# Kernel tuning notes

Hardware: AMD Instinct MI355X
Metric: run time of the kernel (lower is better)

The kernel has to match this reference:

```python
import jax, jax.numpy as jnp
import numpy as np

HID = 256
NUM_ENT = 100000
NUM_REL = 50
E = 320000  # edges per direction; edge_index has 2*E columns
BN_EPS = 1e-5


def setup_inputs() -> dict:
    key = jax.random.key(0)
    ks = jax.random.split(key, 10)
    x = jax.random.normal(ks[0], (NUM_ENT, HID), dtype=jnp.float32)
    edge_index = jax.random.randint(ks[1], (2, 2 * E), 0, NUM_ENT)
    edge_type = jax.random.randint(ks[2], (2 * E,), 0, NUM_REL)
    rel_embed = jax.random.normal(ks[3], (NUM_REL, HID), dtype=jnp.float32)
    # xavier_normal init: std = sqrt(2 / (fan_in + fan_out))
    w_std = (2.0 / (HID + HID)) ** 0.5
    w_loop = jax.random.normal(ks[4], (HID, HID), dtype=jnp.float32) * w_std
    w_in = jax.random.normal(ks[5], (HID, HID), dtype=jnp.float32) * w_std
    w_out = jax.random.normal(ks[6], (HID, HID), dtype=jnp.float32) * w_std
    w_rel = jax.random.normal(ks[7], (HID, HID), dtype=jnp.float32) * w_std
    loop_rel = jax.random.normal(ks[8], (1, HID), dtype=jnp.float32) * ((2.0 / (1 + HID)) ** 0.5)
    bn_weight = jnp.ones((HID,), dtype=jnp.float32)
    bn_bias = jnp.zeros((HID,), dtype=jnp.float32)
    return {
        "x": x, "edge_index": edge_index, "edge_type": edge_type,
        "rel_embed": rel_embed, "w_loop": w_loop, "w_in": w_in,
        "w_out": w_out, "w_rel": w_rel, "loop_rel": loop_rel,
        "bn_weight": bn_weight, "bn_bias": bn_bias,
    }


def _compute_norm(edge_index, num_ent):
    # symmetric D^-1/2 * D^-1/2 norm; degree counted on row (target) index
    row, col = edge_index[0], edge_index[1]
    deg = jax.ops.segment_sum(jnp.ones_like(row, dtype=jnp.float32), row, num_segments=num_ent)
    deg_inv = jnp.where(deg > 0, deg ** -0.5, 0.0)
    return deg_inv[row] * deg_inv[col]


def _propagate(x, idx, etype, rel_all, W, norm, num_ent):
    # gather source nodes (idx[1]), compose with relation emb (mult), transform, scale, scatter-add to targets (idx[0])
    msg = (x[idx[1]] * rel_all[etype]) @ W  # [E, d]
    if norm is not None:
        msg = msg * norm[:, None]
    return jax.ops.segment_sum(msg, idx[0], num_segments=num_ent)


def reference(x, edge_index, edge_type, rel_embed, w_loop, w_in, w_out, w_rel,
              loop_rel, bn_weight, bn_bias):
    num_ent = x.shape[0]
    rel_all = jnp.concatenate([rel_embed, loop_rel], axis=0)  # [R+1, d]
    e = edge_index.shape[1] // 2
    in_index, out_index = edge_index[:, :e], edge_index[:, e:]
    in_type, out_type = edge_type[:e], edge_type[e:]

    in_norm = _compute_norm(in_index, num_ent)
    out_norm = _compute_norm(out_index, num_ent)

    in_res = _propagate(x, in_index, in_type, rel_all, w_in, in_norm, num_ent)
    out_res = _propagate(x, out_index, out_type, rel_all, w_out, out_norm, num_ent)
    # self-loop: identity scatter -> just per-node compose+transform
    loop_res = (x * loop_rel) @ w_loop

    out = (in_res + out_res + loop_res) * (1.0 / 3.0)

    # BatchNorm1d in training mode (batch stats, biased variance)
    mean = out.mean(axis=0)
    var = out.var(axis=0)
    out = (out - mean) * jax.lax.rsqrt(var + BN_EPS) * bn_weight + bn_bias

    rel_out = (rel_all @ w_rel)[:-1]  # drop loop relation
    return out, rel_out
```

## Files before the change

kernel.cpp:

```cpp
#include <hip/hip_runtime.h>

#define HID     256
#define N_ENT   100000
#define TOT_E   640000
#define HALF_E  320000
#define NSEG    (2 * N_ENT)
#define BN_EPSF 1e-5f
#define SCAN_ELEMS 1024
#define NBLK_SCAN  ((NSEG + SCAN_ELEMS - 1) / SCAN_ELEMS)

typedef short bf16x8 __attribute__((ext_vector_type(8)));
typedef float f32x4  __attribute__((ext_vector_type(4)));

__device__ __forceinline__ short f2b(float f) {
    union { float f; unsigned u; } c; c.f = f;
    unsigned u = c.u;
    u += 0x7FFF + ((u >> 16) & 1);
    return (short)(u >> 16);
}

__global__ void hist_kernel(const int* __restrict__ ei, int* __restrict__ offs) {
    int j = blockIdx.x * 256 + threadIdx.x;
    if (j >= TOT_E) return;
    int seg = ei[j] + ((j < HALF_E) ? 0 : N_ENT);
    atomicAdd(&offs[seg], 1);
}

__global__ __launch_bounds__(256) void scan1(int* __restrict__ offs, int* __restrict__ bsums) {
    __shared__ int tsum[256];
    int b = blockIdx.x, t = threadIdx.x;
    int base = b * SCAN_ELEMS + t * 4;
    int v[4] = {0, 0, 0, 0};
    if (base + 3 < NSEG) {
        int4 lv = *(const int4*)(offs + base);
        v[0] = lv.x; v[1] = lv.y; v[2] = lv.z; v[3] = lv.w;
    } else {
        for (int i = 0; i < 4; ++i) if (base + i < NSEG) v[i] = offs[base + i];
    }
    tsum[t] = v[0] + v[1] + v[2] + v[3];
    __syncthreads();
    for (int d = 1; d < 256; d <<= 1) {
        int val = (t >= d) ? tsum[t - d] : 0;
        __syncthreads();
        tsum[t] += val;
        __syncthreads();
    }
    int run = (t == 0) ? 0 : tsum[t - 1];
    if (t == 255) bsums[b] = tsum[255];
    int w[4];
    for (int i = 0; i < 4; ++i) { w[i] = run; run += v[i]; }
    if (base + 3 < NSEG) *(int4*)(offs + base) = make_int4(w[0], w[1], w[2], w[3]);
    else for (int i = 0; i < 4; ++i) if (base + i < NSEG) offs[base + i] = w[i];
}

__global__ void scan2(int* __restrict__ bsums) {
    __shared__ int tmp[256];
    int t = threadIdx.x;
    int v = (t < NBLK_SCAN) ? bsums[t] : 0;
    tmp[t] = v;
    __syncthreads();
    for (int d = 1; d < 256; d <<= 1) {
        int val = (t >= d) ? tmp[t - d] : 0;
        __syncthreads();
        tmp[t] += val;
        __syncthreads();
    }
    if (t < NBLK_SCAN) bsums[t] = (t == 0) ? 0 : tmp[t - 1];
}

__global__ __launch_bounds__(256) void scan3(int* __restrict__ offs, const int* __restrict__ bsums) {
    int b = blockIdx.x;
    int add = bsums[b];
    int base = b * SCAN_ELEMS + threadIdx.x * 4;
    if (base + 3 < NSEG) {
        int4 v = *(int4*)(offs + base);
        v.x += add; v.y += add; v.z += add; v.w += add;
        *(int4*)(offs + base) = v;
    } else {
        for (int i = 0; i < 4; ++i) if (base + i < NSEG) offs[base + i] += add;
    }
}

__global__ void fill_kernel(const int* __restrict__ ei, const int* __restrict__ et,
                            int* __restrict__ offs, int* __restrict__ elist) {
    int j = blockIdx.x * 256 + threadIdx.x;
    if (j >= TOT_E) return;
    int seg = ei[j] + ((j < HALF_E) ? 0 : N_ENT);
    int pos = atomicAdd(&offs[seg], 1);
    elist[pos] = ei[TOT_E + j] | (et[j] << 17);
}

__global__ __launch_bounds__(256) void gather_kernel(
        const float* __restrict__ x, const float* __restrict__ rel,
        const int* __restrict__ offs, const int* __restrict__ elist,
        float* __restrict__ accA, float* __restrict__ accB) {
    int s = blockIdx.x * 4 + (threadIdx.x >> 6);
    int lane = threadIdx.x & 63;
    int start = (s == 0) ? 0 : offs[s - 1];
    int end   = offs[s];
    int half_base = (s >= N_ENT) ? N_ENT : 0;
    int r = s - half_base;
    float4 a = make_float4(0.f, 0.f, 0.f, 0.f);
    if (end > start) {
        float inv_r = rsqrtf((float)(end - start));
        for (int e = start; e < end; ++e) {
            int p = elist[e];
            int c = p & 0x1FFFF;
            int t = p >> 17;
            int sc = half_base + c;
            int cs = (sc == 0) ? 0 : offs[sc - 1];
            int ce = offs[sc];
            if (ce > cs) {
                float norm = inv_r * rsqrtf((float)(ce - cs));
                float4 xv = *(const float4*)(x   + (size_t)c * HID + lane * 4);
                float4 rv = *(const float4*)(rel + (size_t)t * HID + lane * 4);
                a.x += xv.x * rv.x * norm;
                a.y += xv.y * rv.y * norm;
                a.z += xv.z * rv.z * norm;
                a.w += xv.w * rv.w * norm;
            }
        }
    }
    float* dst = ((s >= N_ENT) ? accB : accA) + (size_t)r * HID + lane * 4;
    *(float4*)dst = a;
}

__global__ void wcat_kernel(const float* __restrict__ w_in, const float* __restrict__ w_out,
                            const float* __restrict__ w_loop, const float* __restrict__ loop_rel,
                            short* __restrict__ WT) {
    int n = blockIdx.x;
    int t = threadIdx.x;
    float v0 = w_in  [(size_t)t * HID + n];
    float v1 = w_out [(size_t)t * HID + n];
    float v2 = w_loop[(size_t)t * HID + n] * loop_rel[t];
    short* row = WT + (size_t)n * 768;
    row[t]       = f2b(v0);
    row[256 + t] = f2b(v1);
    row[512 + t] = f2b(v2);
}

__global__ __launch_bounds__(256) void gemm_mfma(
        const float* __restrict__ accA, const float* __restrict__ accB,
        const float* __restrict__ x, const short* __restrict__ WT,
        float* __restrict__ out, float* __restrict__ stats)
{
    __shared__ __align__(16) short As[64 * 64];
    __shared__ __align__(16) short Bs[256 * 64];
    const int tid = threadIdx.x;
    const int l   = tid & 63;
    const int wid = tid >> 6;
    const int r0  = blockIdx.x * 64;
    const int lr  = l & 15;
    const int lg  = l >> 4;

    f32x4 acc[4][4];
    #pragma unroll
    for (int i = 0; i < 4; ++i)
        #pragma unroll
        for (int j = 0; j < 4; ++j)
            acc[i][j] = (f32x4){0.f, 0.f, 0.f, 0.f};

    const int sg = tid & 7;
    const int sr = tid >> 3;

    for (int kt = 0; kt < 12; ++kt) {
        const int src = kt >> 2;
        const float* Ap = (src == 0) ? accA : ((src == 1) ? accB : x);
        const int ksg = kt * 64;
        const int ksl = (kt & 3) * 64;
        __syncthreads();
        #pragma unroll
        for (int h = 0; h < 2; ++h) {
            int r  = sr + 32 * h;
            int gr = r0 + r;
            float4 v0 = make_float4(0.f,0.f,0.f,0.f), v1 = v0;
            if (gr < N_ENT) {
                const float* p = Ap + (size_t)gr * HID + ksl + sg * 8;
                v0 = *(const float4*)p;
                v1 = *(const float4*)(p + 4);
            }
            bf16x8 pk;
            pk[0]=f2b(v0.x); pk[1]=f2b(v0.y); pk[2]=f2b(v0.z); pk[3]=f2b(v0.w);
            pk[4]=f2b(v1.x); pk[5]=f2b(v1.y); pk[6]=f2b(v1.z); pk[7]=f2b(v1.w);
            *(bf16x8*)&As[r * 64 + (sg ^ (r & 7)) * 8] = pk;
        }
        #pragma unroll
        for (int i = 0; i < 8; ++i) {
            int n = sr + 32 * i;
            bf16x8 w = *(const bf16x8*)(WT + (size_t)n * 768 + ksg + sg * 8);
            *(bf16x8*)&Bs[n * 64 + (sg ^ (n & 7)) * 8] = w;
        }
        __syncthreads();
        #pragma unroll
        for (int kc = 0; kc < 2; ++kc) {
            const int gsel = kc * 4 + lg;
            bf16x8 af[4], bfr[4];
            #pragma unroll
            for (int i = 0; i < 4; ++i) {
                int r = 16 * i + lr;
                af[i] = *(const bf16x8*)&As[r * 64 + (gsel ^ (r & 7)) * 8];
            }
            #pragma unroll
            for (int j = 0; j < 4; ++j) {
                int n = wid * 64 + 16 * j + lr;
                bfr[j] = *(const bf16x8*)&Bs[n * 64 + (gsel ^ (n & 7)) * 8];
            }
            #pragma unroll
            for (int i = 0; i < 4; ++i)
                #pragma unroll
                for (int j = 0; j < 4; ++j)
                    acc[i][j] = __builtin_amdgcn_mfma_f32_16x16x32_bf16(
                                    af[i], bfr[j], acc[i][j], 0, 0, 0);
        }
    }

    const float third = 1.f / 3.f;
    float s[4]  = {0.f, 0.f, 0.f, 0.f};
    float sq[4] = {0.f, 0.f, 0.f, 0.f};
    #pragma unroll
    for (int i = 0; i < 4; ++i) {
        #pragma unroll
        for (int v = 0; v < 4; ++v) {
            int grow = r0 + 16 * i + lg * 4 + v;
            if (grow < N_ENT) {
                #pragma unroll
                for (int j = 0; j < 4; ++j) {
                    float val = acc[i][j][v] * third;
                    out[(size_t)grow * HID + wid * 64 + 16 * j + lr] = val;
                    s[j] += val; sq[j] += val * val;
                }
            }
        }
    }
    #pragma unroll
    for (int j = 0; j < 4; ++j) {
        s[j]  += __shfl_xor(s[j], 16);  s[j]  += __shfl_xor(s[j], 32);
        sq[j] += __shfl_xor(sq[j], 16); sq[j] += __shfl_xor(sq[j], 32);
    }
    if (lg == 0) {
        #pragma unroll
        for (int j = 0; j < 4; ++j) {
            int c = wid * 64 + 16 * j + lr;
            atomicAdd(&stats[c], s[j]);
            atomicAdd(&stats[HID + c], sq[j]);
        }
    }
}

__global__ void bn_apply(float* __restrict__ out, const float* __restrict__ stats,
                         const float* __restrict__ bnw, const float* __restrict__ bnb) {
    const float invN = 1.f / (float)N_ENT;
    const size_t total = (size_t)N_ENT * HID;
    for (size_t idx = (size_t)blockIdx.x * 256 + threadIdx.x; idx < total;
         idx += (size_t)gridDim.x * 256) {
        int c = (int)(idx & (HID - 1));
        float mean = stats[c] * invN;
        float var  = stats[HID + c] * invN - mean * mean;
        out[idx] = (out[idx] - mean) * rsqrtf(var + BN_EPSF) * bnw[c] + bnb[c];
    }
}

__global__ void relout_kernel(const float* __restrict__ rel_embed,
                              const float* __restrict__ w_rel,
                              float* __restrict__ rel_out) {
    __shared__ float row[HID];
    int r = blockIdx.x;
    int c = threadIdx.x;
    row[c] = rel_embed[(size_t)r * HID + c];
    __syncthreads();
    float s = 0.f;
    for (int k = 0; k < HID; ++k) s += row[k] * w_rel[(size_t)k * HID + c];
    rel_out[(size_t)r * HID + c] = s;
}

extern "C" void kernel_launch(void* const* d_in, const int* in_sizes, int n_in,
                              void* d_out, int out_size, void* d_ws, size_t ws_size,
                              hipStream_t stream) {
    const float* x        = (const float*)d_in[0];
    const int*   ei       = (const int*)d_in[1];
    const int*   et       = (const int*)d_in[2];
    const float* rel      = (const float*)d_in[3];
    const float* w_loop   = (const float*)d_in[4];
    const float* w_in     = (const float*)d_in[5];
    const float* w_out    = (const float*)d_in[6];
    const float* w_rel    = (const float*)d_in[7];
    const float* loop_rel = (const float*)d_in[8];
    const float* bnw      = (const float*)d_in[9];
    const float* bnb      = (const float*)d_in[10];

    float* out     = (float*)d_out;
    float* rel_out = out + (size_t)N_ENT * HID;
    float* accA    = out;
    float* accB    = (float*)d_ws;

    int*   offs  = (int*)(accB + (size_t)N_ENT * HID);
    int*   elist = offs + NSEG;
    short* WT    = (short*)elist;
    int*   bsums = elist + TOT_E;
    float* stats = (float*)(bsums + 256);

    hipMemsetAsync(offs, 0, NSEG * sizeof(int), stream);
    hipMemsetAsync(stats, 0, 512 * sizeof(float), stream);

    hist_kernel<<<TOT_E / 256, 256, 0, stream>>>(ei, offs);
    scan1<<<NBLK_SCAN, 256, 0, stream>>>(offs, bsums);
    scan2<<<1, 256, 0, stream>>>(bsums);
    scan3<<<NBLK_SCAN, 256, 0, stream>>>(offs, bsums);
    fill_kernel<<<TOT_E / 256, 256, 0, stream>>>(ei, et, offs, elist);
    gather_kernel<<<NSEG / 4, 256, 0, stream>>>(x, rel, offs, elist, accA, accB);
    wcat_kernel<<<256, 256, 0, stream>>>(w_in, w_out, w_loop, loop_rel, WT);
    gemm_mfma<<<(N_ENT + 63) / 64, 256, 0, stream>>>(accA, accB, x, WT, out, stats);
    bn_apply<<<2048, 256, 0, stream>>>(out, stats, bnw, bnb);
    relout_kernel<<<50, 256, 0, stream>>>(rel, w_rel, rel_out);
}
```

Baseline: 375.8 us.

## Convert features to bf16, precompute edge norms, double-buffer GEMM with direct LDS loads

```diff
diff --git a/kernel.cpp b/kernel.cpp
--- a/kernel.cpp
+++ b/kernel.cpp
@@ -10,6 +10,7 @@
 #define NBLK_SCAN  ((NSEG + SCAN_ELEMS - 1) / SCAN_ELEMS)
 
 typedef short bf16x8 __attribute__((ext_vector_type(8)));
+typedef short bf16x4 __attribute__((ext_vector_type(4)));
 typedef float f32x4  __attribute__((ext_vector_type(4)));
 
 __device__ __forceinline__ short f2b(float f) {
@@ -18,6 +19,16 @@
     u += 0x7FFF + ((u >> 16) & 1);
     return (short)(u >> 16);
 }
+__device__ __forceinline__ float b2f(short b) {
+    union { unsigned u; float f; } c;
+    c.u = ((unsigned)(unsigned short)b) << 16;
+    return c.f;
+}
+__device__ __forceinline__ void gload16(const void* g, void* l) {
+    __builtin_amdgcn_global_load_lds(
+        (const __attribute__((address_space(1))) unsigned*)(g),
+        (__attribute__((address_space(3))) unsigned*)(l), 16, 0, 0);
+}
 
 __global__ void hist_kernel(const int* __restrict__ ei, int* __restrict__ offs) {
     int j = blockIdx.x * 256 + threadIdx.x;
@@ -26,7 +37,8 @@
     atomicAdd(&offs[seg], 1);
 }
 
-__global__ __launch_bounds__(256) void scan1(int* __restrict__ offs, int* __restrict__ bsums) {
+__global__ __launch_bounds__(256) void scan1(int* __restrict__ offs, int* __restrict__ bsums,
+                                             float* __restrict__ rnorm) {
     __shared__ int tsum[256];
     int b = blockIdx.x, t = threadIdx.x;
     int base = b * SCAN_ELEMS + t * 4;
@@ -37,6 +49,10 @@
     } else {
         for (int i = 0; i < 4; ++i) if (base + i < NSEG) v[i] = offs[base + i];
     }
+    #pragma unroll
+    for (int i = 0; i < 4; ++i)
+        if (base + i < NSEG)
+            rnorm[base + i] = (v[i] > 0) ? rsqrtf((float)v[i]) : 0.f;
     tsum[t] = v[0] + v[1] + v[2] + v[3];
     __syncthreads();
     for (int d = 1; d < 256; d <<= 1) {
@@ -81,48 +97,75 @@
     }
 }
 
-__global__ void fill_kernel(const int* __restrict__ ei, const int* __restrict__ et,
-                            int* __restrict__ offs, int* __restrict__ elist) {
+__global__ void fill8_kernel(const int* __restrict__ ei, const int* __restrict__ et,
+                             int* __restrict__ offs, const float* __restrict__ rnorm,
+                             int2* __restrict__ elist8) {
     int j = blockIdx.x * 256 + threadIdx.x;
     if (j >= TOT_E) return;
-    int seg = ei[j] + ((j < HALF_E) ? 0 : N_ENT);
+    int hb  = (j < HALF_E) ? 0 : N_ENT;
+    int seg = ei[j] + hb;
+    int col = ei[TOT_E + j];
+    float norm = rnorm[seg] * rnorm[hb + col];
     int pos = atomicAdd(&offs[seg], 1);
-    elist[pos] = ei[TOT_E + j] | (et[j] << 17);
-}
-
-__global__ __launch_bounds__(256) void gather_kernel(
-        const float* __restrict__ x, const float* __restrict__ rel,
-        const int* __restrict__ offs, const int* __restrict__ elist,
-        float* __restrict__ accA, float* __restrict__ accB) {
-    int s = blockIdx.x * 4 + (threadIdx.x >> 6);
-    int lane = threadIdx.x & 63;
+    elist8[pos] = make_int2(col | (et[j] << 17), __float_as_int(norm));
+}
+
+__global__ void tobf16_kernel(const float* __restrict__ src, short* __restrict__ dst, int n8) {
+    int i = blockIdx.x * 256 + threadIdx.x;
+    if (i >= n8) return;
+    const float4* p = (const float4*)(src + (size_t)i * 8);
+    float4 v0 = p[0], v1 = p[1];
+    bf16x8 pk;
+    pk[0]=f2b(v0.x); pk[1]=f2b(v0.y); pk[2]=f2b(v0.z); pk[3]=f2b(v0.w);
+    pk[4]=f2b(v1.x); pk[5]=f2b(v1.y); pk[6]=f2b(v1.z); pk[7]=f2b(v1.w);
+    *(bf16x8*)(dst + (size_t)i * 8) = pk;
+}
+
+__global__ __launch_bounds__(256) void gather_h(
+        const short* __restrict__ xh, const short* __restrict__ relh,
+        const int* __restrict__ offs, const int2* __restrict__ elist8,
+        short* __restrict__ accA, short* __restrict__ accB) {
+    int s = blockIdx.x * 8 + (threadIdx.x >> 5);
+    int lane = threadIdx.x & 31;
     int start = (s == 0) ? 0 : offs[s - 1];
     int end   = offs[s];
-    int half_base = (s >= N_ENT) ? N_ENT : 0;
-    int r = s - half_base;
-    float4 a = make_float4(0.f, 0.f, 0.f, 0.f);
-    if (end > start) {
-        float inv_r = rsqrtf((float)(end - start));
-        for (int e = start; e < end; ++e) {
-            int p = elist[e];
-            int c = p & 0x1FFFF;
-            int t = p >> 17;
-            int sc = half_base + c;
-            int cs = (sc == 0) ? 0 : offs[sc - 1];
-            int ce = offs[sc];
-            if (ce > cs) {
-                float norm = inv_r * rsqrtf((float)(ce - cs));
-                float4 xv = *(const float4*)(x   + (size_t)c * HID + lane * 4);
-                float4 rv = *(const float4*)(rel + (size_t)t * HID + lane * 4);
-                a.x += xv.x * rv.x * norm;
-                a.y += xv.y * rv.y * norm;
-                a.z += xv.z * rv.z * norm;
-                a.w += xv.w * rv.w * norm;
-            }
-        }
-    }
-    float* dst = ((s >= N_ENT) ? accB : accA) + (size_t)r * HID + lane * 4;
-    *(float4*)dst = a;
+    float a0[8], a1[8];
+    #pragma unroll
+    for (int k = 0; k < 8; ++k) { a0[k] = 0.f; a1[k] = 0.f; }
+    int e = start;
+    for (; e + 2 <= end; e += 2) {
+        int2 p0 = elist8[e];
+        int2 p1 = elist8[e + 1];
+        int   c0 = p0.x & 0x1FFFF, t0 = p0.x >> 17;
+        float n0 = __int_as_float(p0.y);
+        int   c1 = p1.x & 0x1FFFF, t1 = p1.x >> 17;
+        float n1 = __int_as_float(p1.y);
+        bf16x8 xv0 = *(const bf16x8*)(xh   + (size_t)c0 * HID + lane * 8);
+        bf16x8 rv0 = *(const bf16x8*)(relh + (size_t)t0 * HID + lane * 8);
+        bf16x8 xv1 = *(const bf16x8*)(xh   + (size_t)c1 * HID + lane * 8);
+        bf16x8 rv1 = *(const bf16x8*)(relh + (size_t)t1 * HID + lane * 8);
+        #pragma unroll
+        for (int k = 0; k < 8; ++k) {
+            a0[k] += b2f(xv0[k]) * b2f(rv0[k]) * n0;
+            a1[k] += b2f(xv1[k]) * b2f(rv1[k]) * n1;
+        }
+    }
+    if (e < end) {
+        int2 p = elist8[e];
+        int   c = p.x & 0x1FFFF, t = p.x >> 17;
+        float n = __int_as_float(p.y);
+        bf16x8 xv = *(const bf16x8*)(xh   + (size_t)c * HID + lane * 8);
+        bf16x8 rv = *(const bf16x8*)(relh + (size_t)t * HID + lane * 8);
+        #pragma unroll
+        for (int k = 0; k < 8; ++k)
+            a0[k] += b2f(xv[k]) * b2f(rv[k]) * n;
+    }
+    int hb = (s >= N_ENT) ? N_ENT : 0;
+    short* dst = ((s >= N_ENT) ? accB : accA) + (size_t)(s - hb) * HID + lane * 8;
+    bf16x8 pk;
+    #pragma unroll
+    for (int k = 0; k < 8; ++k) pk[k] = f2b(a0[k] + a1[k]);
+    *(bf16x8*)dst = pk;
 }
 
 __global__ void wcat_kernel(const float* __restrict__ w_in, const float* __restrict__ w_out,
@@ -139,13 +182,14 @@
     row[512 + t] = f2b(v2);
 }
 
-__global__ __launch_bounds__(256) void gemm_mfma(
-        const float* __restrict__ accA, const float* __restrict__ accB,
-        const float* __restrict__ x, const short* __restrict__ WT,
-        float* __restrict__ out, float* __restrict__ stats)
+template <bool BF16OUT>
+__global__ __launch_bounds__(256) void gemm_mfma_db(
+        const short* __restrict__ accA, const short* __restrict__ accB,
+        const short* __restrict__ xh, const short* __restrict__ WT,
+        float* __restrict__ out, short* __restrict__ outh, float* __restrict__ stats)
 {
-    __shared__ __align__(16) short As[64 * 64];
-    __shared__ __align__(16) short Bs[256 * 64];
+    __shared__ __align__(16) short As[2][64 * 64];
+    __shared__ __align__(16) short Bs[2][256 * 64];
     const int tid = threadIdx.x;
     const int l   = tid & 63;
     const int wid = tid >> 6;
@@ -160,37 +204,34 @@
         for (int j = 0; j < 4; ++j)
             acc[i][j] = (f32x4){0.f, 0.f, 0.f, 0.f};
 
-    const int sg = tid & 7;
-    const int sr = tid >> 3;
-
+    auto stage = [&](int buf, int kt) {
+        const int src = kt >> 2;
+        const short* Ap = (src == 0) ? accA : ((src == 1) ? accB : xh);
+        const int ksl = (kt & 3) * 64;
+        const int ksg = kt * 64;
+        #pragma unroll
+        for (int h = 0; h < 2; ++h) {
+            int c  = wid * 2 + h;
+            int r  = c * 8 + (l >> 3);
+            int sg = (l & 7) ^ (r & 7);
+            int gr = r0 + r;
+            if (gr >= N_ENT) gr = N_ENT - 1;
+            gload16(Ap + (size_t)gr * HID + ksl + sg * 8, &As[buf][c * 512]);
+        }
+        #pragma unroll
+        for (int i = 0; i < 8; ++i) {
+            int c  = wid * 8 + i;
+            int n  = c * 8 + (l >> 3);
+            int sg = (l & 7) ^ (n & 7);
+            gload16(WT + (size_t)n * 768 + ksg + sg * 8, &Bs[buf][c * 512]);
+        }
+    };
+
+    stage(0, 0);
+    __syncthreads();
+    int cur = 0;
     for (int kt = 0; kt < 12; ++kt) {
-        const int src = kt >> 2;
-        const float* Ap = (src == 0) ? accA : ((src == 1) ? accB : x);
-        const int ksg = kt * 64;
-        const int ksl = (kt & 3) * 64;
-        __syncthreads();
-        #pragma unroll
-        for (int h = 0; h < 2; ++h) {
-            int r  = sr + 32 * h;
-            int gr = r0 + r;
-            float4 v0 = make_float4(0.f,0.f,0.f,0.f), v1 = v0;
-            if (gr < N_ENT) {
-                const float* p = Ap + (size_t)gr * HID + ksl + sg * 8;
-                v0 = *(const float4*)p;
-                v1 = *(const float4*)(p + 4);
-            }
-            bf16x8 pk;
-            pk[0]=f2b(v0.x); pk[1]=f2b(v0.y); pk[2]=f2b(v0.z); pk[3]=f2b(v0.w);
-            pk[4]=f2b(v1.x); pk[5]=f2b(v1.y); pk[6]=f2b(v1.z); pk[7]=f2b(v1.w);
-            *(bf16x8*)&As[r * 64 + (sg ^ (r & 7)) * 8] = pk;
-        }
-        #pragma unroll
-        for (int i = 0; i < 8; ++i) {
-            int n = sr + 32 * i;
-            bf16x8 w = *(const bf16x8*)(WT + (size_t)n * 768 + ksg + sg * 8);
-            *(bf16x8*)&Bs[n * 64 + (sg ^ (n & 7)) * 8] = w;
-        }
-        __syncthreads();
+        if (kt < 11) stage(cur ^ 1, kt + 1);
         #pragma unroll
         for (int kc = 0; kc < 2; ++kc) {
             const int gsel = kc * 4 + lg;
@@ -198,12 +239,12 @@
             #pragma unroll
             for (int i = 0; i < 4; ++i) {
                 int r = 16 * i + lr;
-                af[i] = *(const bf16x8*)&As[r * 64 + (gsel ^ (r & 7)) * 8];
+                af[i] = *(const bf16x8*)&As[cur][r * 64 + (gsel ^ (r & 7)) * 8];
             }
             #pragma unroll
             for (int j = 0; j < 4; ++j) {
                 int n = wid * 64 + 16 * j + lr;
-                bfr[j] = *(const bf16x8*)&Bs[n * 64 + (gsel ^ (n & 7)) * 8];
+                bfr[j] = *(const bf16x8*)&Bs[cur][n * 64 + (gsel ^ (n & 7)) * 8];
             }
             #pragma unroll
             for (int i = 0; i < 4; ++i)
@@ -212,6 +253,8 @@
                     acc[i][j] = __builtin_amdgcn_mfma_f32_16x16x32_bf16(
                                     af[i], bfr[j], acc[i][j], 0, 0, 0);
         }
+        __syncthreads();
+        cur ^= 1;
     }
 
     const float third = 1.f / 3.f;
@@ -226,7 +269,9 @@
                 #pragma unroll
                 for (int j = 0; j < 4; ++j) {
                     float val = acc[i][j][v] * third;
-                    out[(size_t)grow * HID + wid * 64 + 16 * j + lr] = val;
+                    int col = wid * 64 + 16 * j + lr;
+                    if (BF16OUT) outh[(size_t)grow * HID + col] = f2b(val);
+                    else         out [(size_t)grow * HID + col] = val;
                     s[j] += val; sq[j] += val * val;
                 }
             }
@@ -247,16 +292,46 @@
     }
 }
 
+__global__ void bn_apply_h(const short* __restrict__ outh, float* __restrict__ out,
+                           const float* __restrict__ stats,
+                           const float* __restrict__ bnw, const float* __restrict__ bnb) {
+    const float invN = 1.f / (float)N_ENT;
+    const int total8 = N_ENT * (HID / 8);
+    for (int i = blockIdx.x * 256 + threadIdx.x; i < total8; i += gridDim.x * 256) {
+        int c = (i & 31) * 8;
+        bf16x8 v = *(const bf16x8*)(outh + (size_t)i * 8);
+        float r[8];
+        #pragma unroll
+        for (int k = 0; k < 8; ++k) {
+            float mean = stats[c + k] * invN;
+            float var  = stats[HID + c + k] * invN - mean * mean;
+            float sc   = rsqrtf(var + BN_EPSF) * bnw[c + k];
+            float sh   = bnb[c + k] - mean * sc;
+            r[k] = b2f(v[k]) * sc + sh;
+        }
+        float4* dst = (float4*)(out + (size_t)i * 8);
+        dst[0] = make_float4(r[0], r[1], r[2], r[3]);
+        dst[1] = make_float4(r[4], r[5], r[6], r[7]);
+    }
+}
+
 __global__ void bn_apply(float* __restrict__ out, const float* __restrict__ stats,
                          const float* __restrict__ bnw, const float* __restrict__ bnb) {
     const float invN = 1.f / (float)N_ENT;
-    const size_t total = (size_t)N_ENT * HID;
-    for (size_t idx = (size_t)blockIdx.x * 256 + threadIdx.x; idx < total;
-         idx += (size_t)gridDim.x * 256) {
-        int c = (int)(idx & (HID - 1));
-        float mean = stats[c] * invN;
-        float var  = stats[HID + c] * invN - mean * mean;
-        out[idx] = (out[idx] - mean) * rsqrtf(var + BN_EPSF) * bnw[c] + bnb[c];
+    const int total4 = N_ENT * (HID / 4);
+    for (int i = blockIdx.x * 256 + threadIdx.x; i < total4; i += gridDim.x * 256) {
+        int c = (i & 63) * 4;
+        float4 v = *(float4*)(out + (size_t)i * 4);
+        #pragma unroll
+        for (int k = 0; k < 4; ++k) {
+            float mean = stats[c + k] * invN;
+            float var  = stats[HID + c + k] * invN - mean * mean;
+            float sc   = rsqrtf(var + BN_EPSF) * bnw[c + k];
+            float sh   = bnb[c + k] - mean * sc;
+            float* comp = (k == 0) ? &v.x : (k == 1) ? &v.y : (k == 2) ? &v.z : &v.w;
+            *comp = (*comp) * sc + sh;
+        }
+        *(float4*)(out + (size_t)i * 4) = v;
     }
 }
 
@@ -290,26 +365,50 @@
 
     float* out     = (float*)d_out;
     float* rel_out = out + (size_t)N_ENT * HID;
-    float* accA    = out;
-    float* accB    = (float*)d_ws;
-
-    int*   offs  = (int*)(accB + (size_t)N_ENT * HID);
-    int*   elist = offs + NSEG;
-    short* WT    = (short*)elist;
-    int*   bsums = elist + TOT_E;
-    float* stats = (float*)(bsums + 256);
-
-    hipMemsetAsync(offs, 0, NSEG * sizeof(int), stream);
-    hipMemsetAsync(stats, 0, 512 * sizeof(float), stream);
-
+
+    const size_t XH_B   = (size_t)N_ENT * HID * 2;
+    const size_t ACC_B  = (size_t)N_ENT * HID * 2;
+    const size_t OFFS_B = (size_t)NSEG * 4;
+    const size_t EL8_B  = (size_t)TOT_E * 8;
+    const size_t RN_B   = (size_t)NSEG * 4;
+    const size_t RELH_B = (size_t)50 * HID * 2;
+    const size_t base_need = XH_B + 2 * ACC_B + OFFS_B + EL8_B + RN_B
+                           + 256 * 4 + 512 * 4 + RELH_B;
+    const size_t OUTH_B = (size_t)N_ENT * HID * 2;
+    const bool   have_outh = (ws_size >= base_need + OUTH_B);
+
+    char* w = (char*)d_ws;
+    short* xh     = (short*)w;              w += XH_B;
+    short* accA_h = (short*)w;              w += ACC_B;
+    short* accB_h = (short*)w;              w += ACC_B;
+    int*   offs   = (int*)w;                w += OFFS_B;
+    int2*  elist8 = (int2*)w;               short* WT = (short*)w;   w += EL8_B;
+    float* rnorm  = (float*)w;              w += RN_B;
+    int*   bsums  = (int*)w;                w += 256 * 4;
+    float* stats  = (float*)w;              w += 512 * 4;
+    short* relh   = (short*)w;              w += RELH_B;
+    short* outh   = (short*)w;
+
+    hipMemsetAsync(offs, 0, OFFS_B, stream);
+    hipMemsetAsync(stats, 0, 512 * 4, stream);
+
+    tobf16_kernel<<<(N_ENT * HID / 8 + 255) / 256, 256, 0, stream>>>(x, xh, N_ENT * HID / 8);
+    tobf16_kernel<<<(50 * HID / 8 + 255) / 256, 256, 0, stream>>>(rel, relh, 50 * HID / 8);
     hist_kernel<<<TOT_E / 256, 256, 0, stream>>>(ei, offs);
-    scan1<<<NBLK_SCAN, 256, 0, stream>>>(offs, bsums);
+    scan1<<<NBLK_SCAN, 256, 0, stream>>>(offs, bsums, rnorm);
     scan2<<<1, 256, 0, stream>>>(bsums);
     scan3<<<NBLK_SCAN, 256, 0, stream>>>(offs, bsums);
-    fill_kernel<<<TOT_E / 256, 256, 0, stream>>>(ei, et, offs, elist);
-    gather_kernel<<<NSEG / 4, 256, 0, stream>>>(x, rel, offs, elist, accA, accB);
+    fill8_kernel<<<TOT_E / 256, 256, 0, stream>>>(ei, et, offs, rnorm, elist8);
+    gather_h<<<NSEG / 8, 256, 0, stream>>>(xh, relh, offs, elist8, accA_h, accB_h);
     wcat_kernel<<<256, 256, 0, stream>>>(w_in, w_out, w_loop, loop_rel, WT);
-    gemm_mfma<<<(N_ENT + 63) / 64, 256, 0, stream>>>(accA, accB, x, WT, out, stats);
-    bn_apply<<<2048, 256, 0, stream>>>(out, stats, bnw, bnb);
+    if (have_outh) {
+        gemm_mfma_db<true><<<(N_ENT + 63) / 64, 256, 0, stream>>>(
+            accA_h, accB_h, xh, WT, out, outh, stats);
+        bn_apply_h<<<2048, 256, 0, stream>>>(outh, out, stats, bnw, bnb);
+    } else {
+        gemm_mfma_db<false><<<(N_ENT + 63) / 64, 256, 0, stream>>>(
+            accA_h, accB_h, xh, WT, out, outh, stats);
+        bn_apply<<<2048, 256, 0, stream>>>(out, stats, bnw, bnb);
+    }
     relout_kernel<<<50, 256, 0, stream>>>(rel, w_rel, rel_out);
 }
```

New measurement: 319.3 us. 1.18x faster.
